# Kernel tuning notes

Hardware: AMD Instinct MI355X
Metric: run time of the kernel (lower is better)

The kernel has to match this reference:

```python
import jax, jax.numpy as jnp
import numpy as np

H = 16        # query heads
HK = 8        # key/value heads
HD = 128      # head dim
EPS = 1e-6
THETA = 1000000.0


def _rmsnorm(x, w):
    # per-head RMSNorm over last dim (head_dim)
    var = jnp.mean(jnp.square(x.astype(jnp.float32)), axis=-1, keepdims=True)
    return (x * jax.lax.rsqrt(var + EPS)).astype(x.dtype) * w


def _rope(x, cos, sin):
    # x: [B, S, h, HD]; cos/sin: [S, HD//2]
    x1, x2 = jnp.split(x, 2, axis=-1)
    c = cos[None, :, None, :]
    s = sin[None, :, None, :]
    return jnp.concatenate([x1 * c - x2 * s, x2 * c + x1 * s], axis=-1)


def setup_inputs() -> dict:
    key = jax.random.key(0)
    ks = jax.random.split(key, 5)
    B, S, D = 2, 2048, 2048
    scale = 0.02
    return {
        "x": jax.random.normal(ks[0], (B, S, D), jnp.float32),
        "wq": jax.random.normal(ks[1], (H * HD, D), jnp.float32) * scale,
        "wk": jax.random.normal(ks[2], (HK * HD, D), jnp.float32) * scale,
        "wv": jax.random.normal(ks[3], (HK * HD, D), jnp.float32) * scale,
        "wo": jax.random.normal(ks[4], (D, H * HD), jnp.float32) * scale,
        "q_norm_w": jnp.ones((HD,), jnp.float32),
        "k_norm_w": jnp.ones((HD,), jnp.float32),
    }


def reference(x, wq, wk, wv, wo, q_norm_w, k_norm_w):
    B, S, D = x.shape
    # QKV projections (no bias)
    q = (x @ wq.T).reshape(B, S, H, HD)
    k = (x @ wk.T).reshape(B, S, HK, HD)
    v = (x @ wv.T).reshape(B, S, HK, HD)

    # per-head RMSNorm on Q and K (Qwen3 qk-norm)
    q = _rmsnorm(q, q_norm_w)
    k = _rmsnorm(k, k_norm_w)

    # RoPE
    inv_freq = 1.0 / (THETA ** (jnp.arange(0, HD, 2, dtype=jnp.float32) / HD))
    ang = jnp.arange(S, dtype=jnp.float32)[:, None] * inv_freq[None, :]  # [S, HD/2]
    cos, sin = jnp.cos(ang), jnp.sin(ang)
    q = _rope(q, cos, sin)
    k = _rope(k, cos, sin)

    # GQA: repeat KV heads to match query heads
    rep = H // HK
    k = jnp.repeat(k, rep, axis=2)  # [B, S, H, HD]
    v = jnp.repeat(v, rep, axis=2)

    # causal SDPA
    scores = jnp.einsum("bqhd,bkhd->bhqk", q, k) / jnp.sqrt(jnp.float32(HD))
    mask = jnp.tril(jnp.ones((S, S), dtype=bool))
    scores = jnp.where(mask[None, None], scores, jnp.finfo(scores.dtype).min)
    probs = jax.nn.softmax(scores, axis=-1)
    out = jnp.einsum("bhqk,bkhd->bqhd", probs, v).reshape(B, S, H * HD)

    return out @ wo.T
```

## Files before the change

### kernel.cpp

```cpp
#include <hip/hip_runtime.h>
#include <hip/hip_bf16.h>
#include <math.h>

#define B_   2
#define S_   2048
#define D_   2048
#define H_   16
#define HK_  8
#define HD_  128
#define BS_  (B_ * S_)
#define NQKV 4096
#define SCALE 0.08838834764831845f

typedef __bf16 bf16x8 __attribute__((ext_vector_type(8)));
typedef __bf16 bf16x4 __attribute__((ext_vector_type(4)));
typedef float  f32x4  __attribute__((ext_vector_type(4)));

#define AS1(p) ((const __attribute__((address_space(1))) void*)(p))
#define AS3(p) ((__attribute__((address_space(3))) void*)(p))

template <int S>
__device__ __forceinline__ float ror16(float x) {
    return __builtin_bit_cast(float, __builtin_amdgcn_update_dpp(
        0, __builtin_bit_cast(int, x), 0x120 | S, 0xF, 0xF, true));
}
__device__ __forceinline__ float row_sum16(float x) {
    x += ror16<8>(x);
    x += ror16<4>(x);
    x += ror16<2>(x);
    x += ror16<1>(x);
    return x;
}

__global__ __launch_bounds__(256) void cvt_all(const float* __restrict__ x,
                                               const float* __restrict__ wq,
                                               const float* __restrict__ wk,
                                               const float* __restrict__ wv,
                                               const float* __restrict__ wo,
                                               __bf16* __restrict__ xb,
                                               __bf16* __restrict__ wb,
                                               __bf16* __restrict__ wob) {
    int bid = blockIdx.x;
    const float* src;
    __bf16* dst;
    int i4;
    if (bid < 8192)       { src = x;  dst = xb;                    i4 = bid * 256; }
    else if (bid < 12288) { src = wq; dst = wb;                    i4 = (bid - 8192) * 256; }
    else if (bid < 14336) { src = wk; dst = wb + (size_t)4194304;  i4 = (bid - 12288) * 256; }
    else if (bid < 16384) { src = wv; dst = wb + (size_t)6291456;  i4 = (bid - 14336) * 256; }
    else                  { src = wo; dst = wob;                   i4 = (bid - 16384) * 256; }
    i4 += threadIdx.x;
    float4 v = reinterpret_cast<const float4*>(src)[i4];
    bf16x4 o = {(__bf16)v.x, (__bf16)v.y, (__bf16)v.z, (__bf16)v.w};
    reinterpret_cast<bf16x4*>(dst)[i4] = o;
}

__global__ __launch_bounds__(128) void build_rope(float* __restrict__ tab) {
    int s = blockIdx.x;
    int d = threadIdx.x;
    int i = d & 63;
    float inv_freq = exp2f(-19.931568569324174f * (float)(2 * i) * (1.0f / 128.0f));
    float ang = (float)s * inv_freq;
    float sn, cs;
    sincosf(ang, &sn, &cs);
    tab[s * 128 + d] = (d < 64) ? cs : sn;
}

__global__ __launch_bounds__(512, 2) void gemm_bf16_8ph(const __bf16* __restrict__ A,
                                                        const __bf16* __restrict__ W,
                                                        __bf16* __restrict__ C,
                                                        int M, int N, int K) {
    __shared__ __bf16 lds[2][2][256 * 64];

    const int t    = threadIdx.x;
    const int w    = t >> 6;
    const int lane = t & 63;
    const int col  = lane & 15;
    const int quad = lane >> 4;
    const int c7   = col & 7;
    const int wm   = w >> 2;
    const int wn   = w & 3;

    const int bid = blockIdx.x;
    const int nid = (bid & 7) * 32 + (bid >> 3);
    const int st  = nid >> 4;
    const int wi  = nid & 15;
    const int m0 = ((st >> 2) * 4 + (wi >> 2)) * 256;
    const int n0 = ((st & 3) * 4 + (wi & 3)) * 256;

    const int lr8 = lane >> 3;
    const int sw8 = ((lane & 7) ^ lr8) * 8;
    const __bf16* Ag = A + (size_t)(m0 + w * 16 + lr8) * K + sw8;
    const __bf16* Wg = W + (size_t)(n0 + w * 16 + lr8) * K + sw8;

    const int nkt = K >> 6;
    const int nit = nkt >> 1;

    const int aBase = (wm * 128 + col) * 64;
    const int bBase = (wn * 64 + col) * 64;
    const int kx0 = (quad ^ c7) * 8;
    const int kx1 = ((4 + quad) ^ c7) * 8;

    f32x4 acc[8][4];
    #pragma unroll
    for (int i = 0; i < 8; i++)
        #pragma unroll
        for (int j = 0; j < 4; j++) acc[i][j] = (f32x4){0.f, 0.f, 0.f, 0.f};

    bf16x8 a[4][2], a2[4][2], b0f[2][2], b1f[2][2];

    auto stg = [&](int ktv, int bufc, int ab, int half) {
        if (ktv >= nkt) return;
        const __bf16* gb = (ab ? Wg : Ag) + (size_t)half * 128 * K + (size_t)ktv * 64;
        __bf16* db = &lds[bufc][ab][(half * 128 + w * 16) * 64];
        __builtin_amdgcn_global_load_lds(AS1(gb), AS3(db), 16, 0, 0);
        __builtin_amdgcn_global_load_lds(AS1(gb + (size_t)8 * K), AS3(db + 512), 16, 0, 0);
    };
    auto lda = [&](bf16x8 (&dst)[4][2], const __bf16* panel, int g) {
        #pragma unroll
        for (int mi = 0; mi < 4; mi++) {
            dst[mi][0] = *reinterpret_cast<const bf16x8*>(&panel[aBase + (g * 64 + mi * 16) * 64 + kx0]);
            dst[mi][1] = *reinterpret_cast<const bf16x8*>(&panel[aBase + (g * 64 + mi * 16) * 64 + kx1]);
        }
    };
    auto ldb = [&](bf16x8 (&dst)[2][2], const __bf16* panel, int ng) {
        #pragma unroll
        for (int ni = 0; ni < 2; ni++) {
            dst[ni][0] = *reinterpret_cast<const bf16x8*>(&panel[bBase + (ng * 32 + ni * 16) * 64 + kx0]);
            dst[ni][1] = *reinterpret_cast<const bf16x8*>(&panel[bBase + (ng * 32 + ni * 16) * 64 + kx1]);
        }
    };
    auto mm = [&](bf16x8 (&af)[4][2], bf16x8 (&bfr)[2][2], int g, int ng) {
        __builtin_amdgcn_s_setprio(1);
        #pragma unroll
        for (int mi = 0; mi < 4; mi++)
            #pragma unroll
            for (int ni = 0; ni < 2; ni++) {
                f32x4 c = acc[g * 4 + mi][ng * 2 + ni];
                c = __builtin_amdgcn_mfma_f32_16x16x32_bf16(af[mi][0], bfr[ni][0], c, 0, 0, 0);
                c = __builtin_amdgcn_mfma_f32_16x16x32_bf16(af[mi][1], bfr[ni][1], c, 0, 0, 0);
                acc[g * 4 + mi][ng * 2 + ni] = c;
            }
        __builtin_amdgcn_s_setprio(0);
    };

#define BAR  __builtin_amdgcn_s_barrier()
#define LGKM(n) do { asm volatile("s_waitcnt lgkmcnt(" #n ")" ::: "memory"); \
                     __builtin_amdgcn_sched_barrier(0); } while (0)
#define VM(n) asm volatile("s_waitcnt vmcnt(" #n ")" ::: "memory")

    const __bf16* P0a = &lds[0][0][0];
    const __bf16* P0b = &lds[0][1][0];
    const __bf16* P1a = &lds[1][0][0];
    const __bf16* P1b = &lds[1][1][0];

    stg(0, 0, 0, 0); stg(0, 0, 0, 1); stg(0, 0, 1, 0); stg(0, 0, 1, 1);
    VM(0);
    BAR;
    lda(a, P0a, 0); ldb(b0f, P0b, 0);

    #pragma unroll 1
    for (int it = 0; it < nit; ++it) {
        const int T1 = it * 2 + 1;

        lda(a2, P0a, 1);
        stg(T1, 1, 0, 0); stg(T1, 1, 0, 1);
        LGKM(8);
        mm(a, b0f, 0, 0);
        ldb(b1f, P0b, 1);
        stg(T1, 1, 1, 0); stg(T1, 1, 1, 1);
        LGKM(4);
        mm(a2, b0f, 1, 0);
        LGKM(0);
        mm(a2, b1f, 1, 1);
        mm(a, b1f, 0, 1);
        VM(0);
        BAR;
        lda(a, P1a, 0); ldb(b0f, P1b, 0);

        lda(a2, P1a, 1);
        stg(T1 + 1, 0, 0, 0); stg(T1 + 1, 0, 0, 1);
        LGKM(8);
        mm(a, b0f, 0, 0);
        ldb(b1f, P1b, 1);
        stg(T1 + 1, 0, 1, 0); stg(T1 + 1, 0, 1, 1);
        LGKM(4);
        mm(a2, b0f, 1, 0);
        LGKM(0);
        mm(a2, b1f, 1, 1);
        mm(a, b1f, 0, 1);
        if (it + 1 < nit) {
            VM(0);
            BAR;
            lda(a, P0a, 0); ldb(b0f, P0b, 0);
        }
    }

#undef BAR
#undef LGKM
#undef VM

    #pragma unroll
    for (int m8 = 0; m8 < 8; m8++) {
        #pragma unroll
        for (int r = 0; r < 4; r++) {
            size_t row = m0 + wm * 128 + m8 * 16 + quad * 4 + r;
            __bf16* cp = C + row * N + n0 + wn * 64 + col;
            #pragma unroll
            for (int n4 = 0; n4 < 4; n4++) cp[n4 * 16] = (__bf16)acc[m8][n4][r];
        }
    }
}

template <typename CT>
__global__ __launch_bounds__(256) void gemm_bf16_nt_n64(const __bf16* __restrict__ A,
                                                        const __bf16* __restrict__ W,
                                                        CT* __restrict__ C,
                                                        int M, int N, int K) {
    __shared__ __bf16 As[128 * 64];
    __shared__ __bf16 Bs[64 * 64];

    const int t    = threadIdx.x;
    const int w    = t >> 6;
    const int lane = t & 63;
    const int col  = lane & 15;
    const int quad = lane >> 4;
    const int wm   = w >> 1;
    const int wn   = w & 1;

    const int m0 = blockIdx.x * 128;
    const int n0 = blockIdx.y * 64;

    const int lrow8 = lane >> 3;
    const int lch   = ((lane & 7) ^ lrow8) * 8;

    const __bf16* agp = A + (size_t)(m0 + w * 32 + lrow8) * K + lch;
    const __bf16* wgp = W + (size_t)(n0 + w * 16 + lrow8) * K + lch;
    __bf16* alp = As + (w * 32) * 64;
    __bf16* blp = Bs + (w * 16) * 64;

    const int c7 = col & 7;

    f32x4 acc[4][2];
    #pragma unroll
    for (int m = 0; m < 4; m++)
        #pragma unroll
        for (int n = 0; n < 2; n++) acc[m][n] = (f32x4){0.f, 0.f, 0.f, 0.f};

    #pragma unroll 1
    for (int k0 = 0; k0 < K; k0 += 64) {
        #pragma unroll
        for (int j = 0; j < 4; j++)
            __builtin_amdgcn_global_load_lds(AS1(agp + k0 + (size_t)(j * 8) * K),
                                             AS3(alp + j * 512), 16, 0, 0);
        #pragma unroll
        for (int j = 0; j < 2; j++)
            __builtin_amdgcn_global_load_lds(AS1(wgp + k0 + (size_t)(j * 8) * K),
                                             AS3(blp + j * 512), 16, 0, 0);
        __syncthreads();

        #pragma unroll
        for (int kk = 0; kk < 2; kk++) {
            bf16x8 af[4], bfr[2];
            #pragma unroll
            for (int m = 0; m < 4; m++)
                af[m] = *reinterpret_cast<const bf16x8*>(
                    &As[(wm * 64 + m * 16 + col) * 64 + ((kk * 4 + quad) ^ c7) * 8]);
            #pragma unroll
            for (int n = 0; n < 2; n++)
                bfr[n] = *reinterpret_cast<const bf16x8*>(
                    &Bs[(wn * 32 + n * 16 + col) * 64 + ((kk * 4 + quad) ^ c7) * 8]);

            #pragma unroll
            for (int m = 0; m < 4; m++)
                #pragma unroll
                for (int n = 0; n < 2; n++)
                    acc[m][n] = __builtin_amdgcn_mfma_f32_16x16x32_bf16(af[m], bfr[n], acc[m][n], 0, 0, 0);
        }
        __syncthreads();
    }

    #pragma unroll
    for (int m = 0; m < 4; m++) {
        #pragma unroll
        for (int r = 0; r < 4; r++) {
            size_t row = m0 + wm * 64 + m * 16 + quad * 4 + r;
            CT* cp = C + row * N + n0 + wn * 32 + col;
            #pragma unroll
            for (int n = 0; n < 2; n++) cp[n * 16] = (CT)acc[m][n][r];
        }
    }
}

__global__ __launch_bounds__(256) void norm_rope(__bf16* __restrict__ qkv,
                                                 const float* __restrict__ qw,
                                                 const float* __restrict__ kw,
                                                 const float* __restrict__ tab) {
    const int g    = blockIdx.x * 16 + (threadIdx.x >> 4);
    const int l    = threadIdx.x & 15;
    const int row  = g / 24;
    const int head = g - row * 24;
    const int s    = row & (S_ - 1);

    const float* w = (head < H_) ? qw : kw;
    __bf16* p = qkv + (size_t)row * NQKV + head * HD_ + l * 8;

    bf16x8 xv = *reinterpret_cast<const bf16x8*>(p);
    float xf[8];
    float ss = 0.f;
    #pragma unroll
    for (int j = 0; j < 8; j++) { xf[j] = (float)xv[j]; ss = fmaf(xf[j], xf[j], ss); }
    ss = row_sum16(ss);
    float rs = rsqrtf(ss * (1.0f / 128.0f) + 1e-6f);

    float nf[8];
    const float4 w0 = *reinterpret_cast<const float4*>(&w[l * 8]);
    const float4 w1 = *reinterpret_cast<const float4*>(&w[l * 8 + 4]);
    nf[0] = xf[0] * rs * w0.x; nf[1] = xf[1] * rs * w0.y;
    nf[2] = xf[2] * rs * w0.z; nf[3] = xf[3] * rs * w0.w;
    nf[4] = xf[4] * rs * w1.x; nf[5] = xf[5] * rs * w1.y;
    nf[6] = xf[6] * rs * w1.z; nf[7] = xf[7] * rs * w1.w;

    float of[8];
    #pragma unroll
    for (int j = 0; j < 8; j++) of[j] = __shfl_xor(nf[j], 8);

    const int ib = (l & 7) * 8;
    const float4 c0 = *reinterpret_cast<const float4*>(&tab[s * 128 + ib]);
    const float4 c1 = *reinterpret_cast<const float4*>(&tab[s * 128 + ib + 4]);
    const float4 s0 = *reinterpret_cast<const float4*>(&tab[s * 128 + 64 + ib]);
    const float4 s1 = *reinterpret_cast<const float4*>(&tab[s * 128 + 64 + ib + 4]);
    float cs[8] = {c0.x, c0.y, c0.z, c0.w, c1.x, c1.y, c1.z, c1.w};
    float sn[8] = {s0.x, s0.y, s0.z, s0.w, s1.x, s1.y, s1.z, s1.w};

    bf16x8 out;
    if (l < 8) {
        #pragma unroll
        for (int j = 0; j < 8; j++) out[j] = (__bf16)(nf[j] * cs[j] - of[j] * sn[j]);
    } else {
        #pragma unroll
        for (int j = 0; j < 8; j++) out[j] = (__bf16)(of[j] * sn[j] + nf[j] * cs[j]);
    }
    *reinterpret_cast<bf16x8*>(p) = out;
}

__global__ __launch_bounds__(256) void transpose_v(const __bf16* __restrict__ qkv,
                                                   __bf16* __restrict__ vt) {
    __shared__ __bf16 Ls[64][136];
    const int t  = threadIdx.x;
    const int bk = blockIdx.y;
    const int b  = bk >> 3;
    const int kvh = bk & 7;
    const int s0 = blockIdx.x * 64;

    #pragma unroll
    for (int i = 0; i < 4; i++) {
        int f = t + i * 256;
        int row = f >> 4;
        int d8 = (f & 15) * 8;
        bf16x8 v = *reinterpret_cast<const bf16x8*>(
            &qkv[(size_t)(b * S_ + s0 + row) * NQKV + 3072 + kvh * HD_ + d8]);
        *reinterpret_cast<bf16x8*>(&Ls[row][d8]) = v;
    }
    __syncthreads();

    #pragma unroll
    for (int i = 0; i < 4; i++) {
        int f = t + i * 256;
        int dim = f >> 3;
        int kc = f & 7;
        bf16x8 o;
        #pragma unroll
        for (int e = 0; e < 8; e++) o[e] = Ls[kc * 8 + e][dim];
        *reinterpret_cast<bf16x8*>(
            &vt[((size_t)bk * HD_ + dim) * S_ + s0 + kc * 8]) = o;
    }
}

__global__ __launch_bounds__(256) void attn_mfma(const __bf16* __restrict__ qkv,
                                                 const __bf16* __restrict__ vt,
                                                 __bf16* __restrict__ ao) {
    __shared__ __align__(16) char smem[17408];
    __bf16 (*Qs)[136] = reinterpret_cast<__bf16(*)[136]>(smem);
    __bf16 (*Ks)[136] = reinterpret_cast<__bf16(*)[136]>(smem);
    __shared__ __bf16 Vt[128][72];
    __shared__ __bf16 Ps[4][16][72];

    const int t    = threadIdx.x;
    const int w    = t >> 6;
    const int lane = t & 63;
    const int col  = lane & 15;
    const int quad = lane >> 4;

    const int bh  = blockIdx.x;
    const int b   = bh >> 4;
    const int h   = bh & 15;
    const int kvh = h >> 1;
    const int qb  = gridDim.y - 1 - blockIdx.y;
    const int r0  = qb * 64;

    const float C0 = SCALE * 1.44269504f;
    const float CM = -12.0f * 1.44269504f;

    const __bf16* vbase = vt + ((size_t)(b * HK_ + kvh) * HD_) * S_;

    const __bf16* kp[4];
    __bf16*       kw_[4];
    const __bf16* vp[4];
    __bf16*       vw_[4];
    #pragma unroll
    for (int i = 0; i < 4; i++) {
        int f = t + i * 256;
        int row = f >> 4, d8 = (f & 15) * 8;
        kp[i]  = qkv + (size_t)(b * S_ + row) * NQKV + 2048 + kvh * HD_ + d8;
        kw_[i] = &Ks[row][d8];
        int dim = f >> 3, kc = f & 7;
        vp[i]  = vbase + (size_t)dim * S_ + kc * 8;
        vw_[i] = &Vt[dim][kc * 8];
    }

    bf16x8 kreg[4], vreg[4];
    #pragma unroll
    for (int i = 0; i < 4; i++) {
        kreg[i] = *reinterpret_cast<const bf16x8*>(kp[i]);  kp[i] += (size_t)64 * NQKV;
        vreg[i] = *reinterpret_cast<const bf16x8*>(vp[i]);  vp[i] += 64;
    }

    #pragma unroll
    for (int i = 0; i < 4; i++) {
        int f   = t + i * 256;
        int row = f >> 4;
        int d8  = (f & 15) * 8;
        bf16x8 v = *reinterpret_cast<const bf16x8*>(
            &qkv[(size_t)(b * S_ + r0 + row) * NQKV + h * HD_ + d8]);
        *reinterpret_cast<bf16x8*>(&Qs[row][d8]) = v;
    }
    __syncthreads();

    bf16x8 qf[4];
    {
        const int m = w * 16 + col;
        #pragma unroll
        for (int k = 0; k < 4; k++)
            qf[k] = *reinterpret_cast<const bf16x8*>(&Qs[m][k * 32 + quad * 8]);
    }

    f32x4 o_acc[8];
    #pragma unroll
    for (int i = 0; i < 8; i++) o_acc[i] = (f32x4){0.f, 0.f, 0.f, 0.f};
    float l_lane[4] = {0.f, 0.f, 0.f, 0.f};

    const int ntiles = qb + 1;
    for (int ti = 0; ti < ntiles; ti++) {
        __syncthreads();

        #pragma unroll
        for (int i = 0; i < 4; i++) {
            *reinterpret_cast<bf16x8*>(kw_[i]) = kreg[i];
            *reinterpret_cast<bf16x8*>(vw_[i]) = vreg[i];
        }
        if (ti + 1 < ntiles) {
            #pragma unroll
            for (int i = 0; i < 4; i++) {
                kreg[i] = *reinterpret_cast<const bf16x8*>(kp[i]);  kp[i] += (size_t)64 * NQKV;
                vreg[i] = *reinterpret_cast<const bf16x8*>(vp[i]);  vp[i] += 64;
            }
        }
        __syncthreads();

        f32x4 s[4];
        #pragma unroll
        for (int n = 0; n < 4; n++) {
            f32x4 acc = (f32x4){0.f, 0.f, 0.f, 0.f};
            #pragma unroll
            for (int k = 0; k < 4; k++) {
                bf16x8 bf = *reinterpret_cast<const bf16x8*>(
                    &Ks[n * 16 + col][k * 32 + quad * 8]);
                acc = __builtin_amdgcn_mfma_f32_16x16x32_bf16(qf[k], bf, acc, 0, 0, 0);
            }
            s[n] = acc;
        }

        const bool diag = (ti == qb);
        #pragma unroll
        for (int r = 0; r < 4; r++) {
            float p0 = exp2f(fmaf(s[0][r], C0, CM));
            float p1 = exp2f(fmaf(s[1][r], C0, CM));
            float p2 = exp2f(fmaf(s[2][r], C0, CM));
            float p3 = exp2f(fmaf(s[3][r], C0, CM));
            if (diag) {
                int qloc = w * 16 + quad * 4 + r;
                if (0 * 16 + col > qloc) p0 = 0.f;
                if (1 * 16 + col > qloc) p1 = 0.f;
                if (2 * 16 + col > qloc) p2 = 0.f;
                if (3 * 16 + col > qloc) p3 = 0.f;
            }
            l_lane[r] += p0 + p1 + p2 + p3;
            Ps[w][quad * 4 + r][0 * 16 + col] = (__bf16)p0;
            Ps[w][quad * 4 + r][1 * 16 + col] = (__bf16)p1;
            Ps[w][quad * 4 + r][2 * 16 + col] = (__bf16)p2;
            Ps[w][quad * 4 + r][3 * 16 + col] = (__bf16)p3;
        }

        bf16x8 pf[2];
        #pragma unroll
        for (int ks = 0; ks < 2; ks++)
            pf[ks] = *reinterpret_cast<const bf16x8*>(&Ps[w][col][ks * 32 + quad * 8]);
        #pragma unroll
        for (int n = 0; n < 8; n++) {
            #pragma unroll
            for (int ks = 0; ks < 2; ks++) {
                bf16x8 vf = *reinterpret_cast<const bf16x8*>(
                    &Vt[n * 16 + col][ks * 32 + quad * 8]);
                o_acc[n] = __builtin_amdgcn_mfma_f32_16x16x32_bf16(pf[ks], vf, o_acc[n], 0, 0, 0);
            }
        }
    }

    #pragma unroll
    for (int r = 0; r < 4; r++) {
        float l = row_sum16(l_lane[r]);
        float inv = 1.0f / l;
        int qrow = r0 + w * 16 + quad * 4 + r;
        __bf16* op = ao + (size_t)(b * S_ + qrow) * (H_ * HD_) + h * HD_ + col;
        #pragma unroll
        for (int n = 0; n < 8; n++)
            op[n * 16] = (__bf16)(o_acc[n][r] * inv);
    }
}

extern "C" void kernel_launch(void* const* d_in, const int* in_sizes, int n_in,
                              void* d_out, int out_size, void* d_ws, size_t ws_size,
                              hipStream_t stream) {
    const float* x  = (const float*)d_in[0];
    const float* wq = (const float*)d_in[1];
    const float* wk = (const float*)d_in[2];
    const float* wv = (const float*)d_in[3];
    const float* wo = (const float*)d_in[4];
    const float* qw = (const float*)d_in[5];
    const float* kw = (const float*)d_in[6];
    float* out = (float*)d_out;

    __bf16* ws  = (__bf16*)d_ws;
    __bf16* xb  = ws;
    __bf16* wb  = xb  + (size_t)8388608;
    __bf16* wob = wb  + (size_t)8388608;
    __bf16* qkv = wob + (size_t)4194304;
    __bf16* ao  = qkv + (size_t)16777216;
    __bf16* vtg = ao  + (size_t)8388608;
    float* rtab = (float*)ao;

    cvt_all<<<20480, 256, 0, stream>>>(x, wq, wk, wv, wo, xb, wb, wob);
    build_rope<<<S_, 128, 0, stream>>>(rtab);

    gemm_bf16_8ph<<<256, 512, 0, stream>>>(xb, wb, qkv, BS_, NQKV, D_);

    norm_rope<<<(BS_ * 24) / 16, 256, 0, stream>>>(qkv, qw, kw, rtab);

    transpose_v<<<dim3(S_ / 64, B_ * HK_), 256, 0, stream>>>(qkv, vtg);

    attn_mfma<<<dim3(B_ * H_, S_ / 64), 256, 0, stream>>>(qkv, vtg, ao);

    gemm_bf16_nt_n64<float><<<dim3(BS_ / 128, D_ / 64), 256, 0, stream>>>(
        ao, wob, out, BS_, D_, H_ * HD_);
}
```

Measured before the change: 351.2 us.

## Restructure GEMM main loop with deeper staggered global-to-LDS prefetch

```diff
diff --git a/kernel.cpp b/kernel.cpp
--- a/kernel.cpp
+++ b/kernel.cpp
@@ -144,10 +144,11 @@
         __builtin_amdgcn_s_setprio(0);
     };
 
-#define BAR  __builtin_amdgcn_s_barrier()
-#define LGKM(n) do { asm volatile("s_waitcnt lgkmcnt(" #n ")" ::: "memory"); \
-                     __builtin_amdgcn_sched_barrier(0); } while (0)
-#define VM(n) asm volatile("s_waitcnt vmcnt(" #n ")" ::: "memory")
+#define BAR   __builtin_amdgcn_s_barrier()
+#define LG0   asm volatile("s_waitcnt lgkmcnt(0)" ::: "memory")
+#define LG8   asm volatile("s_waitcnt lgkmcnt(8)" ::: "memory")
+#define VM6   asm volatile("s_waitcnt vmcnt(6)" ::: "memory")
+#define VM0   asm volatile("s_waitcnt vmcnt(0)" ::: "memory")
 
     const __bf16* P0a = &lds[0][0][0];
     const __bf16* P0b = &lds[0][1][0];
@@ -155,50 +156,67 @@
     const __bf16* P1b = &lds[1][1][0];
 
     stg(0, 0, 0, 0); stg(0, 0, 0, 1); stg(0, 0, 1, 0); stg(0, 0, 1, 1);
-    VM(0);
+    stg(1, 1, 0, 0); stg(1, 1, 0, 1); stg(1, 1, 1, 0);
+    VM6;
     BAR;
-    lda(a, P0a, 0); ldb(b0f, P0b, 0);
 
     #pragma unroll 1
     for (int it = 0; it < nit; ++it) {
         const int T1 = it * 2 + 1;
-
+        const int T2 = it * 2 + 2;
+        const int T3 = it * 2 + 3;
+        const bool last = (it == nit - 1);
+
+        lda(a, P0a, 0); ldb(b0f, P0b, 0);
+        stg(T1, 1, 1, 1);
+        LG8;
+        BAR; LG0;
+        mm(a, b0f, 0, 0);
+        BAR;
         lda(a2, P0a, 1);
-        stg(T1, 1, 0, 0); stg(T1, 1, 0, 1);
-        LGKM(8);
+        stg(T2, 0, 0, 0);
+        BAR; LG0;
+        mm(a2, b0f, 1, 0);
+        BAR;
+        ldb(b1f, P0b, 1);
+        stg(T2, 0, 0, 1);
+        BAR; LG0;
+        mm(a2, b1f, 1, 1);
+        BAR;
+        stg(T2, 0, 1, 0);
+        BAR;
+        mm(a, b1f, 0, 1);
+        if (last) { VM0; } else { VM6; }
+        BAR;
+
+        lda(a, P1a, 0); ldb(b0f, P1b, 0);
+        stg(T2, 0, 1, 1);
+        LG8;
+        BAR; LG0;
         mm(a, b0f, 0, 0);
-        ldb(b1f, P0b, 1);
-        stg(T1, 1, 1, 0); stg(T1, 1, 1, 1);
-        LGKM(4);
+        BAR;
+        lda(a2, P1a, 1);
+        stg(T3, 1, 0, 0);
+        BAR; LG0;
         mm(a2, b0f, 1, 0);
-        LGKM(0);
+        BAR;
+        ldb(b1f, P1b, 1);
+        stg(T3, 1, 0, 1);
+        BAR; LG0;
         mm(a2, b1f, 1, 1);
+        BAR;
+        stg(T3, 1, 1, 0);
+        BAR;
         mm(a, b1f, 0, 1);
-        VM(0);
-        BAR;
-        lda(a, P1a, 0); ldb(b0f, P1b, 0);
-
-        lda(a2, P1a, 1);
-        stg(T1 + 1, 0, 0, 0); stg(T1 + 1, 0, 0, 1);
-        LGKM(8);
-        mm(a, b0f, 0, 0);
-        ldb(b1f, P1b, 1);
-        stg(T1 + 1, 0, 1, 0); stg(T1 + 1, 0, 1, 1);
-        LGKM(4);
-        mm(a2, b0f, 1, 0);
-        LGKM(0);
-        mm(a2, b1f, 1, 1);
-        mm(a, b1f, 0, 1);
-        if (it + 1 < nit) {
-            VM(0);
-            BAR;
-            lda(a, P0a, 0); ldb(b0f, P0b, 0);
-        }
+        if (!last) { VM6; }
+        BAR;
     }
 
 #undef BAR
-#undef LGKM
-#undef VM
+#undef LG0
+#undef LG8
+#undef VM6
+#undef VM0
 
     #pragma unroll
     for (int m8 = 0; m8 < 8; m8++) {
```

New measurement: 336.5 us. 1.04x faster.
